# Kernel optimization log

Measured on AMD Instinct MI355X. Metric: run time of the kernel, lower is better.

## Reference

```python
import jax, jax.numpy as jnp
import numpy as np

B, N = 64, 65536


def setup_inputs() -> dict:
    key = jax.random.key(0)
    k1, k2, k3 = jax.random.split(key, 3)
    src = jax.random.normal(k1, (B, 3, N), dtype=jnp.float32)
    tgt = jax.random.normal(k2, (B, 3, N), dtype=jnp.float32)
    w = jax.random.uniform(k3, (B, N), dtype=jnp.float32)
    # soft-correspondence weights sum to 1 over points (matches intended use;
    # math below is faithful regardless of normalization)
    weights = w / jnp.sum(w, axis=1, keepdims=True)
    return {"src": src, "tgt": tgt, "weights": weights}


def reference(src, tgt, weights):
    # src, tgt: [B, 3, N]; weights: [B, N]
    src_t = jnp.swapaxes(src, 1, 2)  # [B, N, 3]
    tgt_t = jnp.swapaxes(tgt, 1, 2)  # [B, N, 3]
    # weighted centroids (w^T @ X), [B, 3]
    srcm = jnp.einsum('bn,bnc->bc', weights, src_t)
    tgtm = jnp.einsum('bn,bnc->bc', weights, tgt_t)
    src_c = src_t - srcm[:, None, :]  # [B, N, 3]
    tgt_c = tgt_t - tgtm[:, None, :]  # [B, N, 3]
    # H = Xc^T diag(w) Yc, computed without the O(N^2) diag_embed -> [B, 3, 3]
    H = jnp.einsum('bni,bn,bnj->bij', src_c, weights, tgt_c)
    U, S, Vt = jnp.linalg.svd(H)
    V = jnp.swapaxes(Vt, -1, -2)
    Ut = jnp.swapaxes(U, -1, -2)
    R0 = jnp.matmul(V, Ut)  # [B, 3, 3]
    det = jnp.linalg.det(R0)  # [B]
    # Kabsch reflection fix: if det(R) < 0, flip 3rd column of V (V @ diag(1,1,-1))
    sign = jnp.where(det < 0, -1.0, 1.0).astype(H.dtype)  # [B]
    ones = jnp.ones_like(sign)
    col_scale = jnp.stack([ones, ones, sign], axis=-1)  # [B, 3]
    R = jnp.matmul(V * col_scale[:, None, :], Ut)  # [B, 3, 3]
    # t = -R @ srcm + tgtm -> [B, 3]
    t = tgtm - jnp.einsum('bij,bj->bi', R, srcm)
    return (R, t)
```

## Files before the change

### kernel.cpp

```cpp
#include <hip/hip_runtime.h>
#include <math.h>

#define B_BATCH 64
#define N_PTS   65536
#define BPB     32
#define THREADS 256
#define CHUNK   (N_PTS / BPB)
#define TILES   (CHUNK / 4 / THREADS)

typedef float floatx4 __attribute__((ext_vector_type(4)));

__global__ __launch_bounds__(THREADS) void partial_sums(
        const float* __restrict__ src, const float* __restrict__ tgt,
        const float* __restrict__ w,  float* __restrict__ part) {
    const int xcd   = blockIdx.x & 7;
    const int local = blockIdx.x >> 3;
    const int b     = xcd * 8 + (local & 7);
    const int blk   = local >> 3;
    const int n0    = blk * CHUNK;
    const int t     = threadIdx.x;

    const floatx4* wp = (const floatx4*)(w   + (size_t)b * N_PTS          + n0);
    const floatx4* s0 = (const floatx4*)(src + ((size_t)b*3 + 0) * N_PTS + n0);
    const floatx4* s1 = (const floatx4*)(src + ((size_t)b*3 + 1) * N_PTS + n0);
    const floatx4* s2 = (const floatx4*)(src + ((size_t)b*3 + 2) * N_PTS + n0);
    const floatx4* t0 = (const floatx4*)(tgt + ((size_t)b*3 + 0) * N_PTS + n0);
    const floatx4* t1 = (const floatx4*)(tgt + ((size_t)b*3 + 1) * N_PTS + n0);
    const floatx4* t2 = (const floatx4*)(tgt + ((size_t)b*3 + 2) * N_PTS + n0);

    float a[16];
#pragma unroll
    for (int k = 0; k < 16; ++k) a[k] = 0.0f;

#define ACC1(WW, X0, X1, X2, Y0, Y1, Y2) { \
    float ww = WW; \
    float ws0 = ww * X0, ws1 = ww * X1, ws2 = ww * X2; \
    a[0]  += ww; \
    a[1]  += ws0;       a[2]  += ws1;       a[3]  += ws2; \
    a[4]  += ww * Y0;   a[5]  += ww * Y1;   a[6]  += ww * Y2; \
    a[7]  += ws0 * Y0;  a[8]  += ws0 * Y1;  a[9]  += ws0 * Y2; \
    a[10] += ws1 * Y0;  a[11] += ws1 * Y1;  a[12] += ws1 * Y2; \
    a[13] += ws2 * Y0;  a[14] += ws2 * Y1;  a[15] += ws2 * Y2; }

#pragma unroll
    for (int tt = 0; tt < TILES; ++tt) {
        const int idx = tt * THREADS + t;
        floatx4 wv = __builtin_nontemporal_load(&wp[idx]);
        floatx4 x0 = __builtin_nontemporal_load(&s0[idx]);
        __builtin_amdgcn_s_waitcnt(0);
        floatx4 x1 = __builtin_nontemporal_load(&s1[idx]);
        floatx4 x2 = __builtin_nontemporal_load(&s2[idx]);
        __builtin_amdgcn_s_waitcnt(0);
        floatx4 y0 = __builtin_nontemporal_load(&t0[idx]);
        floatx4 y1 = __builtin_nontemporal_load(&t1[idx]);
        __builtin_amdgcn_s_waitcnt(0);
        floatx4 y2 = __builtin_nontemporal_load(&t2[idx]);
        __builtin_amdgcn_s_waitcnt(0);
#pragma unroll
        for (int c = 0; c < 4; ++c) {
            ACC1(wv[c], x0[c], x1[c], x2[c], y0[c], y1[c], y2[c])
        }
    }
#undef ACC1

    const int lane = t & 63;
    const int wave = t >> 6;
    __shared__ float lds[4][16];
#pragma unroll
    for (int k = 0; k < 16; ++k) {
        float v = a[k];
        v += __shfl_down(v, 32);
        v += __shfl_down(v, 16);
        v += __shfl_down(v, 8);
        v += __shfl_down(v, 4);
        v += __shfl_down(v, 2);
        v += __shfl_down(v, 1);
        if (lane == 0) lds[wave][k] = v;
    }
    __syncthreads();
    if (t < 16) {
        float v = lds[0][t] + lds[1][t] + lds[2][t] + lds[3][t];
        part[(size_t)(b * BPB + blk) * 16 + t] = v;
    }
}

__global__ __launch_bounds__(64) void finalize(
        const float* __restrict__ part, float* __restrict__ out) {
    const int b = blockIdx.x;
    const int l = threadIdx.x;

    float a[16];
    if (l < BPB) {
        const float4* p = (const float4*)(part + (size_t)(b * BPB + l) * 16);
        float4 q0 = p[0], q1 = p[1], q2 = p[2], q3 = p[3];
        a[0]=q0.x; a[1]=q0.y; a[2]=q0.z; a[3]=q0.w;
        a[4]=q1.x; a[5]=q1.y; a[6]=q1.z; a[7]=q1.w;
        a[8]=q2.x; a[9]=q2.y; a[10]=q2.z; a[11]=q2.w;
        a[12]=q3.x; a[13]=q3.y; a[14]=q3.z; a[15]=q3.w;
    } else {
#pragma unroll
        for (int k = 0; k < 16; ++k) a[k] = 0.0f;
    }
#pragma unroll
    for (int k = 0; k < 16; ++k) {
        float v = a[k];
        v += __shfl_down(v, 32);
        v += __shfl_down(v, 16);
        v += __shfl_down(v, 8);
        v += __shfl_down(v, 4);
        v += __shfl_down(v, 2);
        v += __shfl_down(v, 1);
        a[k] = v;
    }
    if (l != 0) return;

    float W = a[0];
    float A[3]  = {a[1], a[2], a[3]};
    float Bv[3] = {a[4], a[5], a[6]};
    float H[3][3];
#pragma unroll
    for (int i = 0; i < 3; ++i)
#pragma unroll
        for (int j = 0; j < 3; ++j)
            H[i][j] = a[7 + i*3 + j] + (W - 2.0f) * A[i] * Bv[j];

    float fn = 0.0f;
    for (int i = 0; i < 3; ++i) for (int j = 0; j < 3; ++j) fn += H[i][j]*H[i][j];
    fn = sqrtf(fn);
    float inv = (fn > 1e-30f) ? 1.0f/fn : 1.0f;
    float h[3][3];
    for (int i = 0; i < 3; ++i) for (int j = 0; j < 3; ++j) h[i][j] = H[i][j]*inv;

    float M[3][3];
    for (int i = 0; i < 3; ++i)
        for (int j = 0; j < 3; ++j) {
            float s = 0.0f;
            for (int k = 0; k < 3; ++k) s += h[k][i] * h[k][j];
            M[i][j] = s;
        }

    float V[3][3] = {{1,0,0},{0,1,0},{0,0,1}};
    const int PAIRS[3][2] = {{0,1},{0,2},{1,2}};
    for (int sweep = 0; sweep < 12; ++sweep) {
        float off = M[0][1]*M[0][1] + M[0][2]*M[0][2] + M[1][2]*M[1][2];
        if (off < 1e-14f) break;
        for (int pp = 0; pp < 3; ++pp) {
            const int pq = PAIRS[pp][0], qq = PAIRS[pp][1];
            float apq = M[pq][qq];
            if (fabsf(apq) < 1e-30f) continue;
            float tau = (M[qq][qq] - M[pq][pq]) / (2.0f * apq);
            float t = (tau >= 0.0f ? 1.0f : -1.0f) / (fabsf(tau) + sqrtf(1.0f + tau*tau));
            float c = 1.0f / sqrtf(1.0f + t*t), s = t * c;
            for (int k = 0; k < 3; ++k) {
                float mkp = M[k][pq], mkq = M[k][qq];
                M[k][pq] = c*mkp - s*mkq;
                M[k][qq] = s*mkp + c*mkq;
            }
            for (int k = 0; k < 3; ++k) {
                float mpk = M[pq][k], mqk = M[qq][k];
                M[pq][k] = c*mpk - s*mqk;
                M[qq][k] = s*mpk + c*mqk;
            }
            for (int k = 0; k < 3; ++k) {
                float vkp = V[k][pq], vkq = V[k][qq];
                V[k][pq] = c*vkp - s*vkq;
                V[k][qq] = s*vkp + c*vkq;
            }
        }
    }

    float e[3] = {M[0][0], M[1][1], M[2][2]};
    int idx[3] = {0, 1, 2};
    if (e[idx[0]] < e[idx[1]]) { int t_ = idx[0]; idx[0] = idx[1]; idx[1] = t_; }
    if (e[idx[0]] < e[idx[2]]) { int t_ = idx[0]; idx[0] = idx[2]; idx[2] = t_; }
    if (e[idx[1]] < e[idx[2]]) { int t_ = idx[1]; idx[1] = idx[2]; idx[2] = t_; }
    float Vc[3][3];
    for (int i = 0; i < 3; ++i)
        for (int k = 0; k < 3; ++k) Vc[i][k] = V[i][idx[k]];

    float u[3][3], hv[3][3];
    for (int k = 0; k < 3; ++k)
        for (int j = 0; j < 3; ++j) {
            float s = 0.0f;
            for (int m = 0; m < 3; ++m) s += h[j][m] * Vc[m][k];
            hv[k][j] = s;
        }
    float n1 = sqrtf(hv[0][0]*hv[0][0] + hv[0][1]*hv[0][1] + hv[0][2]*hv[0][2]);
    float in1 = (n1 > 1e-20f) ? 1.0f/n1 : 0.0f;
    for (int j = 0; j < 3; ++j) u[0][j] = hv[0][j] * in1;
    if (in1 == 0.0f) { u[0][0] = 1.0f; u[0][1] = 0.0f; u[0][2] = 0.0f; }
    float d12 = u[0][0]*hv[1][0] + u[0][1]*hv[1][1] + u[0][2]*hv[1][2];
    float w2[3];
    for (int j = 0; j < 3; ++j) w2[j] = hv[1][j] - d12 * u[0][j];
    float n2 = sqrtf(w2[0]*w2[0] + w2[1]*w2[1] + w2[2]*w2[2]);
    if (n2 > 1e-20f) {
        for (int j = 0; j < 3; ++j) u[1][j] = w2[j] / n2;
    } else {
        float ax = fabsf(u[0][0]), ay = fabsf(u[0][1]), az = fabsf(u[0][2]);
        float t2[3];
        if (ax <= ay && ax <= az)      { t2[0]=0; t2[1]=-u[0][2]; t2[2]=u[0][1]; }
        else if (ay <= az)             { t2[0]=-u[0][2]; t2[1]=0; t2[2]=u[0][0]; }
        else                           { t2[0]=-u[0][1]; t2[1]=u[0][0]; t2[2]=0; }
        float nt = sqrtf(t2[0]*t2[0] + t2[1]*t2[1] + t2[2]*t2[2]);
        for (int j = 0; j < 3; ++j) u[1][j] = t2[j] / nt;
    }
    u[2][0] = u[0][1]*u[1][2] - u[0][2]*u[1][1];
    u[2][1] = u[0][2]*u[1][0] - u[0][0]*u[1][2];
    u[2][2] = u[0][0]*u[1][1] - u[0][1]*u[1][0];

    float R[3][3];
    for (int i = 0; i < 3; ++i)
        for (int j = 0; j < 3; ++j) {
            float s = 0.0f;
            for (int k = 0; k < 3; ++k) s += Vc[i][k] * u[k][j];
            R[i][j] = s;
        }
    float det = R[0][0]*(R[1][1]*R[2][2] - R[1][2]*R[2][1])
              - R[0][1]*(R[1][0]*R[2][2] - R[1][2]*R[2][0])
              + R[0][2]*(R[1][0]*R[2][1] - R[1][1]*R[2][0]);
    if (det < 0.0f)
        for (int i = 0; i < 3; ++i)
            for (int j = 0; j < 3; ++j)
                R[i][j] -= 2.0f * Vc[i][2] * u[2][j];

    float tv[3];
    for (int i = 0; i < 3; ++i)
        tv[i] = Bv[i] - (R[i][0]*A[0] + R[i][1]*A[1] + R[i][2]*A[2]);

    for (int i = 0; i < 3; ++i)
        for (int j = 0; j < 3; ++j)
            out[b*9 + i*3 + j] = R[i][j];
    for (int i = 0; i < 3; ++i)
        out[B_BATCH*9 + b*3 + i] = tv[i];
}

extern "C" void kernel_launch(void* const* d_in, const int* in_sizes, int n_in,
                              void* d_out, int out_size, void* d_ws, size_t ws_size,
                              hipStream_t stream) {
    const float* src = (const float*)d_in[0];
    const float* tgt = (const float*)d_in[1];
    const float* w   = (const float*)d_in[2];
    float* out  = (float*)d_out;
    float* part = (float*)d_ws;

    partial_sums<<<B_BATCH * BPB, THREADS, 0, stream>>>(src, tgt, w, part);
    finalize<<<B_BATCH, 64, 0, stream>>>(part, out);
}
```

Before: 148.6 us.

## Stage streams through LDS with per-wave producer loads and larger blocks

The kernel drops the per-thread loads of all seven streams, which were serialized by explicit waitcnt barriers. Blocks now have 512 threads, and each of seven waves loads one stream (weights, src x/y/z, tgt x/y/z) into a 56KB shared buffer with eight outstanding vector loads per lane. All eight waves then compute the 16 accumulators from LDS. Blocks per batch go from 32 to 8, aiming for more memory parallelism per wave. The cost is two barriers per iteration, no overlap between the load and compute phases, and lower occupancy from the large LDS footprint.

```diff
diff --git a/kernel.cpp b/kernel.cpp
--- a/kernel.cpp
+++ b/kernel.cpp
@@ -3,10 +3,11 @@
 
 #define B_BATCH 64
 #define N_PTS   65536
-#define BPB     32
-#define THREADS 256
+#define BPB     8
+#define THREADS 512
 #define CHUNK   (N_PTS / BPB)
-#define TILES   (CHUNK / 4 / THREADS)
+#define P_ITER  2048
+#define ITERS   (CHUNK / P_ITER)
 
 typedef float floatx4 __attribute__((ext_vector_type(4)));
 
@@ -19,14 +20,23 @@
     const int blk   = local >> 3;
     const int n0    = blk * CHUNK;
     const int t     = threadIdx.x;
-
-    const floatx4* wp = (const floatx4*)(w   + (size_t)b * N_PTS          + n0);
-    const floatx4* s0 = (const floatx4*)(src + ((size_t)b*3 + 0) * N_PTS + n0);
-    const floatx4* s1 = (const floatx4*)(src + ((size_t)b*3 + 1) * N_PTS + n0);
-    const floatx4* s2 = (const floatx4*)(src + ((size_t)b*3 + 2) * N_PTS + n0);
-    const floatx4* t0 = (const floatx4*)(tgt + ((size_t)b*3 + 0) * N_PTS + n0);
-    const floatx4* t1 = (const floatx4*)(tgt + ((size_t)b*3 + 1) * N_PTS + n0);
-    const floatx4* t2 = (const floatx4*)(tgt + ((size_t)b*3 + 2) * N_PTS + n0);
+    const int lane  = t & 63;
+    const int wave  = t >> 6;
+
+    const float* gbase = nullptr;
+    switch (wave) {
+        case 0: gbase = w   + (size_t)b * N_PTS          + n0; break;
+        case 1: gbase = src + ((size_t)b*3 + 0) * N_PTS + n0; break;
+        case 2: gbase = src + ((size_t)b*3 + 1) * N_PTS + n0; break;
+        case 3: gbase = src + ((size_t)b*3 + 2) * N_PTS + n0; break;
+        case 4: gbase = tgt + ((size_t)b*3 + 0) * N_PTS + n0; break;
+        case 5: gbase = tgt + ((size_t)b*3 + 1) * N_PTS + n0; break;
+        case 6: gbase = tgt + ((size_t)b*3 + 2) * N_PTS + n0; break;
+        default: break;
+    }
+
+    __shared__ float sm[7 * P_ITER];
+    __shared__ float red[8][16];
 
     float a[16];
 #pragma unroll
@@ -42,30 +52,33 @@
     a[10] += ws1 * Y0;  a[11] += ws1 * Y1;  a[12] += ws1 * Y2; \
     a[13] += ws2 * Y0;  a[14] += ws2 * Y1;  a[15] += ws2 * Y2; }
 
-#pragma unroll
-    for (int tt = 0; tt < TILES; ++tt) {
-        const int idx = tt * THREADS + t;
-        floatx4 wv = __builtin_nontemporal_load(&wp[idx]);
-        floatx4 x0 = __builtin_nontemporal_load(&s0[idx]);
-        __builtin_amdgcn_s_waitcnt(0);
-        floatx4 x1 = __builtin_nontemporal_load(&s1[idx]);
-        floatx4 x2 = __builtin_nontemporal_load(&s2[idx]);
-        __builtin_amdgcn_s_waitcnt(0);
-        floatx4 y0 = __builtin_nontemporal_load(&t0[idx]);
-        floatx4 y1 = __builtin_nontemporal_load(&t1[idx]);
-        __builtin_amdgcn_s_waitcnt(0);
-        floatx4 y2 = __builtin_nontemporal_load(&t2[idx]);
-        __builtin_amdgcn_s_waitcnt(0);
-#pragma unroll
-        for (int c = 0; c < 4; ++c) {
-            ACC1(wv[c], x0[c], x1[c], x2[c], y0[c], y1[c], y2[c])
-        }
+    for (int it = 0; it < ITERS; ++it) {
+        if (wave < 7) {
+            const floatx4* g = (const floatx4*)(gbase + it * P_ITER);
+            floatx4* d = (floatx4*)&sm[wave * P_ITER];
+#pragma unroll
+            for (int j = 0; j < 8; ++j) {
+                d[lane + 64*j] = __builtin_nontemporal_load(&g[lane + 64*j]);
+            }
+        }
+        __syncthreads();
+        {
+            floatx4 wv = ((const floatx4*)&sm[0 * P_ITER])[t];
+            floatx4 x0 = ((const floatx4*)&sm[1 * P_ITER])[t];
+            floatx4 x1 = ((const floatx4*)&sm[2 * P_ITER])[t];
+            floatx4 x2 = ((const floatx4*)&sm[3 * P_ITER])[t];
+            floatx4 y0 = ((const floatx4*)&sm[4 * P_ITER])[t];
+            floatx4 y1 = ((const floatx4*)&sm[5 * P_ITER])[t];
+            floatx4 y2 = ((const floatx4*)&sm[6 * P_ITER])[t];
+#pragma unroll
+            for (int c = 0; c < 4; ++c) {
+                ACC1(wv[c], x0[c], x1[c], x2[c], y0[c], y1[c], y2[c])
+            }
+        }
+        __syncthreads();
     }
 #undef ACC1
 
-    const int lane = t & 63;
-    const int wave = t >> 6;
-    __shared__ float lds[4][16];
 #pragma unroll
     for (int k = 0; k < 16; ++k) {
         float v = a[k];
@@ -75,11 +88,12 @@
         v += __shfl_down(v, 4);
         v += __shfl_down(v, 2);
         v += __shfl_down(v, 1);
-        if (lane == 0) lds[wave][k] = v;
+        if (lane == 0) red[wave][k] = v;
     }
     __syncthreads();
     if (t < 16) {
-        float v = lds[0][t] + lds[1][t] + lds[2][t] + lds[3][t];
+        float v = red[0][t] + red[1][t] + red[2][t] + red[3][t]
+                + red[4][t] + red[5][t] + red[6][t] + red[7][t];
         part[(size_t)(b * BPB + blk) * 16 + t] = v;
     }
 }
```

New measurement: 143.5 us. 3.4% less time.
